# Performance work log

Hardware: AMD Instinct MI355X
Metric: run time of the kernel (lower is better)

Reference implementation:

```python
import jax, jax.numpy as jnp
import numpy as np

EMBED_DIM = 1024
NUM_HEADS = 16
HEAD_DIM = EMBED_DIM // NUM_HEADS


def setup_inputs() -> dict:
    key = jax.random.key(0)
    ks = jax.random.split(key, 10)
    B, S, D = 4, 2048, EMBED_DIM
    s = 1.0 / np.sqrt(D)
    return {
        "x": jax.random.normal(ks[0], (B, S, D), dtype=jnp.float32),
        "Wq": jax.random.normal(ks[1], (D, D), dtype=jnp.float32) * s,
        "bq": jnp.zeros((D,), dtype=jnp.float32),
        "Wk": jax.random.normal(ks[2], (D, D), dtype=jnp.float32) * s,
        "bk": jnp.zeros((D,), dtype=jnp.float32),
        "Wv": jax.random.normal(ks[3], (D, D), dtype=jnp.float32) * s,
        "bv": jnp.zeros((D,), dtype=jnp.float32),
        "Wo": jax.random.normal(ks[4], (D, D), dtype=jnp.float32) * s,
        "bo": jnp.zeros((D,), dtype=jnp.float32),
        "ln_w": jnp.ones((D,), dtype=jnp.float32),
        "ln_b": jnp.zeros((D,), dtype=jnp.float32),
    }


def _layernorm(x, w, b, eps=1e-5):
    mu = jnp.mean(x, axis=-1, keepdims=True)
    var = jnp.mean(jnp.square(x - mu), axis=-1, keepdims=True)
    return (x - mu) * jax.lax.rsqrt(var + eps) * w + b


def reference(x, Wq, bq, Wk, bk, Wv, bv, Wo, bo, ln_w, ln_b):
    B, S, D = x.shape
    H, hd = NUM_HEADS, HEAD_DIM
    # projections (torch Linear: x @ W.T + b)
    q = (x @ Wq.T + bq).reshape(B, S, H, hd).transpose(0, 2, 1, 3)  # [B,H,S,hd]
    k = (x @ Wk.T + bk).reshape(B, S, H, hd).transpose(0, 2, 1, 3)
    v = (x @ Wv.T + bv).reshape(B, S, H, hd).transpose(0, 2, 1, 3)
    scores = jnp.einsum("bhqd,bhkd->bhqk", q, k) / np.sqrt(hd)
    attn = jax.nn.softmax(scores, axis=-1)
    out = jnp.einsum("bhqk,bhkd->bhqd", attn, v)
    out = out.transpose(0, 2, 1, 3).reshape(B, S, D)
    out = out @ Wo.T + bo
    return _layernorm(out, ln_w, ln_b)
```

## Files before the change

kernel.cpp:

```cpp
#include <hip/hip_runtime.h>
#include <hip/hip_bf16.h>
#include <math.h>

typedef unsigned short u16;
typedef unsigned int   u32;
typedef short bf16x8 __attribute__((ext_vector_type(8)));
typedef float f32x4  __attribute__((ext_vector_type(4)));
typedef float f32x16 __attribute__((ext_vector_type(16)));
typedef u32   u32x4  __attribute__((ext_vector_type(4)));
typedef u32   u32x2  __attribute__((ext_vector_type(2)));

#define B_   4
#define S_   2048
#define D_   1024
#define H_   16
#define HD_  64
#define M_   (B_*S_)

static __device__ __forceinline__ u16 f2bf(float f) {
  __hip_bfloat16 h = __float2bfloat16(f);
  return *reinterpret_cast<u16*>(&h);
}
static __device__ __forceinline__ u32 pack_bf(float lo, float hi) {
  return (u32)f2bf(lo) | ((u32)f2bf(hi) << 16);
}
static __device__ __forceinline__ u32 pack_bf_trunc(float lo, float hi) {
  return __builtin_amdgcn_perm(__float_as_uint(hi), __float_as_uint(lo), 0x07060302u);
}
static __device__ __forceinline__ f32x16 zero16() {
  f32x16 z;
#pragma unroll
  for (int i = 0; i < 16; ++i) z[i] = 0.f;
  return z;
}

typedef __attribute__((address_space(1))) const u32* gas_t;
typedef __attribute__((address_space(3))) u32* las_t;
static __device__ __forceinline__ void g2l16(const void* g, void* l) {
  __builtin_amdgcn_global_load_lds((gas_t)g, (las_t)l, 16, 0, 0);
}

__global__ __launch_bounds__(256) void cast_all(const float* __restrict__ x,
                                                const float* __restrict__ Wq,
                                                const float* __restrict__ Wk,
                                                const float* __restrict__ Wv,
                                                const float* __restrict__ Wo,
                                                u16* __restrict__ xb,
                                                u16* __restrict__ Wqb,
                                                u16* __restrict__ Wkb,
                                                u16* __restrict__ Wvb,
                                                u16* __restrict__ Wob) {
  int bid = blockIdx.x;
  const float* src;
  u16* dst;
  int off;
  if (bid < 8192) {
    src = x; dst = xb; off = bid;
  } else {
    int t = bid - 8192;
    int w = t >> 10;
    off   = t & 1023;
    src = w == 0 ? Wq : w == 1 ? Wk : w == 2 ? Wv : Wo;
    dst = w == 0 ? Wqb : w == 1 ? Wkb : w == 2 ? Wvb : Wob;
  }
  int i = (off * 256 + threadIdx.x) * 4;
  float4 v = *reinterpret_cast<const float4*>(src + i);
  uint2 o;
  o.x = pack_bf(v.x, v.y);
  o.y = pack_bf(v.z, v.w);
  *reinterpret_cast<uint2*>(dst + i) = o;
}

__global__ __launch_bounds__(256) void gemm_qkv(const u16* __restrict__ A,
                                                const u16* __restrict__ Wq,
                                                const u16* __restrict__ Wk,
                                                const u16* __restrict__ Wv,
                                                const float* __restrict__ bq,
                                                const float* __restrict__ bk,
                                                const float* __restrict__ bv,
                                                u16* __restrict__ Qo,
                                                u16* __restrict__ Ko,
                                                u16* __restrict__ Vo) {
  const int tid  = threadIdx.x;
  const int lane = tid & 63;
  const int wave = tid >> 6;
  const int m16  = lane & 15;
  const int quad = lane >> 4;
  const int wm   = wave & 1;
  const int wn   = wave >> 1;
  const int which = blockIdx.x % 3;
  const int m0   = (blockIdx.x / 3) * 128;
  const int n0   = blockIdx.y * 128;

  const u16* W = which == 0 ? Wq : which == 1 ? Wk : Wv;
  const float* bias = which == 0 ? bq : which == 1 ? bk : bv;

  __shared__ __align__(16) u16 As[128 * 32];
  __shared__ __align__(16) u16 Bs[128 * 32];

  f32x4 acc[4][4];
#pragma unroll
  for (int i = 0; i < 4; ++i)
#pragma unroll
    for (int j = 0; j < 4; ++j) acc[i][j] = (f32x4){0.f, 0.f, 0.f, 0.f};

  for (int k0 = 0; k0 < 1024; k0 += 32) {
#pragma unroll
    for (int i = 0; i < 2; ++i) {
      int e0  = i * 256 + (wave << 6);
      int e   = e0 + lane;
      int row = e >> 2;
      int c8  = (e & 3) * 8;
      g2l16(&A[(size_t)(m0 + row) * 1024 + k0 + c8], &As[e0 * 8]);
      g2l16(&W[(size_t)(n0 + row) * 1024 + k0 + c8], &Bs[e0 * 8]);
    }
    __syncthreads();

    bf16x8 af[4], bfr[4];
#pragma unroll
    for (int mt = 0; mt < 4; ++mt)
      af[mt] = *reinterpret_cast<const bf16x8*>(&As[(wm * 64 + mt * 16 + m16) * 32 + quad * 8]);
#pragma unroll
    for (int nt = 0; nt < 4; ++nt)
      bfr[nt] = *reinterpret_cast<const bf16x8*>(&Bs[(wn * 64 + nt * 16 + m16) * 32 + quad * 8]);

#pragma unroll
    for (int mt = 0; mt < 4; ++mt)
#pragma unroll
      for (int nt = 0; nt < 4; ++nt)
        acc[mt][nt] = __builtin_amdgcn_mfma_f32_16x16x32_bf16(af[mt], bfr[nt], acc[mt][nt], 0, 0, 0);
    __syncthreads();
  }

  const float scale = which == 0 ? 0.125f * 1.44269504f : 1.0f;
  u16* ob = which == 0 ? Qo : which == 1 ? Ko : Vo;
#pragma unroll
  for (int mt = 0; mt < 4; ++mt) {
#pragma unroll
    for (int nt = 0; nt < 4; ++nt) {
      int col = n0 + wn * 64 + nt * 16 + m16;
      float bi = bias[col];
      int row0 = m0 + wm * 64 + mt * 16 + quad * 4;
      int b = row0 >> 11, s = row0 & 2047;
      int h = col >> 6,  d = col & 63;
      float v[4];
#pragma unroll
      for (int r = 0; r < 4; ++r) v[r] = (acc[mt][nt][r] + bi) * scale;
      if (which < 2) {
#pragma unroll
        for (int r = 0; r < 4; ++r)
          ob[(size_t)((b * H_ + h) * S_ + s + r) * HD_ + d] = f2bf(v[r]);
      } else {
        uint2 w;
        w.x = pack_bf(v[0], v[1]);
        w.y = pack_bf(v[2], v[3]);
        *reinterpret_cast<uint2*>(&ob[(size_t)((b * H_ + h) * HD_ + d) * S_ + s]) = w;
      }
    }
  }
}

__global__ __launch_bounds__(256) void gemm_bt(const u16* __restrict__ A,
                                               const u16* __restrict__ W,
                                               const float* __restrict__ bias,
                                               float* __restrict__ out) {
  const int tid  = threadIdx.x;
  const int lane = tid & 63;
  const int wave = tid >> 6;
  const int m16  = lane & 15;
  const int quad = lane >> 4;
  const int wm   = wave & 1;
  const int wn   = wave >> 1;
  const int m0   = blockIdx.x * 128;
  const int n0   = blockIdx.y * 128;

  __shared__ __align__(16) u16 As[128 * 32];
  __shared__ __align__(16) u16 Bs[128 * 32];

  f32x4 acc[4][4];
#pragma unroll
  for (int i = 0; i < 4; ++i)
#pragma unroll
    for (int j = 0; j < 4; ++j) acc[i][j] = (f32x4){0.f, 0.f, 0.f, 0.f};

  for (int k0 = 0; k0 < 1024; k0 += 32) {
#pragma unroll
    for (int i = 0; i < 2; ++i) {
      int e0  = i * 256 + (wave << 6);
      int e   = e0 + lane;
      int row = e >> 2;
      int c8  = (e & 3) * 8;
      g2l16(&A[(size_t)(m0 + row) * 1024 + k0 + c8], &As[e0 * 8]);
      g2l16(&W[(size_t)(n0 + row) * 1024 + k0 + c8], &Bs[e0 * 8]);
    }
    __syncthreads();

    bf16x8 af[4], bfr[4];
#pragma unroll
    for (int mt = 0; mt < 4; ++mt)
      af[mt] = *reinterpret_cast<const bf16x8*>(&As[(wm * 64 + mt * 16 + m16) * 32 + quad * 8]);
#pragma unroll
    for (int nt = 0; nt < 4; ++nt)
      bfr[nt] = *reinterpret_cast<const bf16x8*>(&Bs[(wn * 64 + nt * 16 + m16) * 32 + quad * 8]);

#pragma unroll
    for (int mt = 0; mt < 4; ++mt)
#pragma unroll
      for (int nt = 0; nt < 4; ++nt)
        acc[mt][nt] = __builtin_amdgcn_mfma_f32_16x16x32_bf16(af[mt], bfr[nt], acc[mt][nt], 0, 0, 0);
    __syncthreads();
  }

#pragma unroll
  for (int mt = 0; mt < 4; ++mt) {
#pragma unroll
    for (int nt = 0; nt < 4; ++nt) {
      int col = n0 + wn * 64 + nt * 16 + m16;
      float bi = bias[col];
#pragma unroll
      for (int r = 0; r < 4; ++r) {
        int row = m0 + wm * 64 + mt * 16 + quad * 4 + r;
        out[(size_t)row * 1024 + col] = acc[mt][nt][r] + bi;
      }
    }
  }
}

__global__ __launch_bounds__(256, 4) void attn_kernel(const u16* __restrict__ Q,
                                                      const u16* __restrict__ K,
                                                      const u16* __restrict__ Vt,
                                                      u16* __restrict__ out) {
  const int tid  = threadIdx.x;
  const int lane = tid & 63;
  const int wave = tid >> 6;
  const int r32  = lane & 31;
  const int h32  = lane >> 5;
  const int bh   = blockIdx.y;
  const int q0   = blockIdx.x * 128 + wave * 32;

  __shared__ __align__(16) u16 Ks[2][64 * 72];
  __shared__ __align__(16) u16 Vs[2][64 * 72];

  const u16* kbase = K  + (size_t)bh * S_ * HD_;
  const u16* vbase = Vt + (size_t)bh * HD_ * S_;
  const int e  = tid;
  const int e2 = tid + 256;
  const int row_a = e >> 3,  c8_a = (e & 7) * 8;
  const int row_b = e2 >> 3, c8_b = (e2 & 7) * 8;

  bf16x8 qf[4];
  {
    const u16* qbase = Q + (size_t)(bh * S_ + q0 + r32) * HD_ + h32 * 8;
#pragma unroll
    for (int dc = 0; dc < 4; ++dc)
      qf[dc] = *reinterpret_cast<const bf16x8*>(qbase + dc * 16);
  }

  f32x16 acc[2];
#pragma unroll
  for (int dt = 0; dt < 2; ++dt) acc[dt] = zero16();
  float lsum = 0.f;

  uint4 kr0 = *reinterpret_cast<const uint4*>(&kbase[(size_t)row_a * HD_ + c8_a]);
  uint4 kr1 = *reinterpret_cast<const uint4*>(&kbase[(size_t)row_b * HD_ + c8_b]);
  uint4 vr0 = *reinterpret_cast<const uint4*>(&vbase[(size_t)row_a * S_ + c8_a]);
  uint4 vr1 = *reinterpret_cast<const uint4*>(&vbase[(size_t)row_b * S_ + c8_b]);

  const int NT = S_ / 64;
  for (int kt = 0; kt < NT; ++kt) {
    u16* ks = Ks[kt & 1];
    u16* vs = Vs[kt & 1];
    *reinterpret_cast<uint4*>(&ks[row_a * 72 + c8_a]) = kr0;
    *reinterpret_cast<uint4*>(&ks[row_b * 72 + c8_b]) = kr1;
    *reinterpret_cast<uint4*>(&vs[row_a * 72 + c8_a]) = vr0;
    *reinterpret_cast<uint4*>(&vs[row_b * 72 + c8_b]) = vr1;
    __syncthreads();

    {
      const int kn = (kt + 1 < NT ? kt + 1 : kt) * 64;
      kr0 = *reinterpret_cast<const uint4*>(&kbase[(size_t)(kn + row_a) * HD_ + c8_a]);
      kr1 = *reinterpret_cast<const uint4*>(&kbase[(size_t)(kn + row_b) * HD_ + c8_b]);
      vr0 = *reinterpret_cast<const uint4*>(&vbase[(size_t)row_a * S_ + kn + c8_a]);
      vr1 = *reinterpret_cast<const uint4*>(&vbase[(size_t)row_b * S_ + kn + c8_b]);
    }

    f32x16 sc[2];
    __builtin_amdgcn_s_setprio(1);
#pragma unroll
    for (int nt = 0; nt < 2; ++nt) {
      sc[nt] = zero16();
#pragma unroll
      for (int dc = 0; dc < 4; ++dc) {
        bf16x8 kf = *reinterpret_cast<const bf16x8*>(&ks[(nt * 32 + r32) * 72 + dc * 16 + h32 * 8]);
        sc[nt] = __builtin_amdgcn_mfma_f32_32x32x16_bf16(kf, qf[dc], sc[nt], 0, 0, 0);
      }
    }
    __builtin_amdgcn_s_setprio(0);

    u32 pk[2][8];
    float ps0 = 0.f, ps1 = 0.f;
#pragma unroll
    for (int nt = 0; nt < 2; ++nt)
#pragma unroll
      for (int i = 0; i < 8; ++i) {
        float p0 = __builtin_amdgcn_exp2f(sc[nt][2 * i]);
        float p1 = __builtin_amdgcn_exp2f(sc[nt][2 * i + 1]);
        ps0 += p0;
        ps1 += p1;
        pk[nt][i] = pack_bf_trunc(p0, p1);
      }
    lsum += ps0 + ps1;

    __builtin_amdgcn_s_setprio(1);
#pragma unroll
    for (int nt = 0; nt < 2; ++nt) {
#pragma unroll
      for (int kc2 = 0; kc2 < 2; ++kc2) {
        u32x2 r0 = __builtin_amdgcn_permlane32_swap(pk[nt][4 * kc2 + 0], pk[nt][4 * kc2 + 2], false, false);
        u32x2 r1 = __builtin_amdgcn_permlane32_swap(pk[nt][4 * kc2 + 1], pk[nt][4 * kc2 + 3], false, false);
        u32x4 bw;
        bw[0] = r0[0];
        bw[1] = r1[0];
        bw[2] = r0[1];
        bw[3] = r1[1];
        bf16x8 pfrag = *reinterpret_cast<bf16x8*>(&bw);
        const int kc = nt * 2 + kc2;
#pragma unroll
        for (int dt = 0; dt < 2; ++dt) {
          bf16x8 vf = *reinterpret_cast<const bf16x8*>(&vs[(dt * 32 + r32) * 72 + kc * 16 + h32 * 8]);
          acc[dt] = __builtin_amdgcn_mfma_f32_32x32x16_bf16(vf, pfrag, acc[dt], 0, 0, 0);
        }
      }
    }
    __builtin_amdgcn_s_setprio(0);
  }

  const int b = bh >> 4, hh = bh & 15;
  float lt  = lsum + __shfl_xor(lsum, 32);
  float inv = 1.f / lt;
  int srow = q0 + r32;
  u16* orow = out + (size_t)(b * S_ + srow) * D_ + hh * HD_;
#pragma unroll
  for (int dt = 0; dt < 2; ++dt) {
#pragma unroll
    for (int g = 0; g < 4; ++g) {
      uint2 w;
      w.x = pack_bf(acc[dt][4 * g + 0] * inv, acc[dt][4 * g + 1] * inv);
      w.y = pack_bf(acc[dt][4 * g + 2] * inv, acc[dt][4 * g + 3] * inv);
      *reinterpret_cast<uint2*>(orow + dt * 32 + 8 * g + 4 * h32) = w;
    }
  }
}

__global__ __launch_bounds__(256) void ln_kernel(const float* __restrict__ X,
                                                 const float* __restrict__ w,
                                                 const float* __restrict__ b,
                                                 float* __restrict__ out) {
  const int row = blockIdx.x;
  const int tid = threadIdx.x;
  const float* x = X + (size_t)row * 1024;
  float vals[4];
  float s = 0.f, s2 = 0.f;
#pragma unroll
  for (int i = 0; i < 4; ++i) {
    float v = x[tid + i * 256];
    vals[i] = v;
    s += v;
    s2 += v * v;
  }
#pragma unroll
  for (int off = 32; off; off >>= 1) {
    s  += __shfl_xor(s, off);
    s2 += __shfl_xor(s2, off);
  }
  __shared__ float a1[4], a2[4];
  if ((tid & 63) == 0) { a1[tid >> 6] = s; a2[tid >> 6] = s2; }
  __syncthreads();
  s  = a1[0] + a1[1] + a1[2] + a1[3];
  s2 = a2[0] + a2[1] + a2[2] + a2[3];
  float mu  = s * (1.f / 1024.f);
  float var = s2 * (1.f / 1024.f) - mu * mu;
  float inv = rsqrtf(var + 1e-5f);
#pragma unroll
  for (int i = 0; i < 4; ++i) {
    int c = tid + i * 256;
    out[(size_t)row * 1024 + c] = (vals[i] - mu) * inv * w[c] + b[c];
  }
}

extern "C" void kernel_launch(void* const* d_in, const int* in_sizes, int n_in,
                              void* d_out, int out_size, void* d_ws, size_t ws_size,
                              hipStream_t stream) {
  const float* x   = (const float*)d_in[0];
  const float* Wq  = (const float*)d_in[1];
  const float* bq  = (const float*)d_in[2];
  const float* Wk  = (const float*)d_in[3];
  const float* bk  = (const float*)d_in[4];
  const float* Wv  = (const float*)d_in[5];
  const float* bv  = (const float*)d_in[6];
  const float* Wo  = (const float*)d_in[7];
  const float* bo  = (const float*)d_in[8];
  const float* lnw = (const float*)d_in[9];
  const float* lnb = (const float*)d_in[10];

  const size_t MB = 1024ull * 1024ull;
  char* ws = (char*)d_ws;
  u16* xb  = (u16*)(ws + 0);
  u16* Qb  = (u16*)(ws + 16 * MB);
  u16* Kb  = (u16*)(ws + 32 * MB);
  u16* Vtb = (u16*)(ws + 48 * MB);
  u16* Wqb = (u16*)(ws + 64 * MB);
  u16* Wkb = (u16*)(ws + 66 * MB);
  u16* Wvb = (u16*)(ws + 68 * MB);
  u16* Wob = (u16*)(ws + 70 * MB);
  float* Of = (float*)(ws + 16 * MB);

  cast_all<<<8192 + 4096, 256, 0, stream>>>(x, Wq, Wk, Wv, Wo, xb, Wqb, Wkb, Wvb, Wob);

  gemm_qkv<<<dim3((M_ / 128) * 3, D_ / 128), 256, 0, stream>>>(
      xb, Wqb, Wkb, Wvb, bq, bk, bv, Qb, Kb, Vtb);

  attn_kernel<<<dim3(S_ / 128, B_ * H_), 256, 0, stream>>>(Qb, Kb, Vtb, xb);

  gemm_bt<<<dim3(M_ / 128, D_ / 128), 256, 0, stream>>>(xb, Wob, bo, Of);

  ln_kernel<<<M_, 256, 0, stream>>>(Of, lnw, lnb, (float*)d_out);
}
```

Measured before the change: 304.5 us.

## Double-buffer GEMM LDS tiles and swizzle block order for XCD locality

Both projection GEMMs now use two LDS buffers, so the global-to-LDS copy of the next K tile is issued before computing on the current one, overlapping loads with MFMA work and dropping one barrier per iteration. All three kernels switch to 1D grids with a block-index swizzle (bid&7 striding), which groups neighbouring tiles onto the same XCD to improve L2 reuse of A/W and K/V. This doubles LDS use in the GEMMs, which may reduce occupancy.

Result: slower. 320.9 us (+5.4%).

```diff
diff --git a/kernel.cpp b/kernel.cpp
--- a/kernel.cpp
+++ b/kernel.cpp
@@ -88,15 +88,21 @@
   const int quad = lane >> 4;
   const int wm   = wave & 1;
   const int wn   = wave >> 1;
-  const int which = blockIdx.x % 3;
-  const int m0   = (blockIdx.x / 3) * 128;
-  const int n0   = blockIdx.y * 128;
+
+  const int bid = blockIdx.x;
+  const int swz = (bid & 7) * 192 + (bid >> 3);
+  const int m_   = swz / 24;
+  const int rr   = swz % 24;
+  const int which = rr >> 3;
+  const int nb   = rr & 7;
+  const int m0   = m_ * 128;
+  const int n0   = nb * 128;
 
   const u16* W = which == 0 ? Wq : which == 1 ? Wk : Wv;
   const float* bias = which == 0 ? bq : which == 1 ? bk : bv;
 
-  __shared__ __align__(16) u16 As[128 * 32];
-  __shared__ __align__(16) u16 Bs[128 * 32];
+  __shared__ __align__(16) u16 As[2][128 * 32];
+  __shared__ __align__(16) u16 Bs[2][128 * 32];
 
   f32x4 acc[4][4];
 #pragma unroll
@@ -104,25 +110,33 @@
 #pragma unroll
     for (int j = 0; j < 4; ++j) acc[i][j] = (f32x4){0.f, 0.f, 0.f, 0.f};
 
-  for (int k0 = 0; k0 < 1024; k0 += 32) {
-#pragma unroll
-    for (int i = 0; i < 2; ++i) {
-      int e0  = i * 256 + (wave << 6);
-      int e   = e0 + lane;
-      int row = e >> 2;
-      int c8  = (e & 3) * 8;
-      g2l16(&A[(size_t)(m0 + row) * 1024 + k0 + c8], &As[e0 * 8]);
-      g2l16(&W[(size_t)(n0 + row) * 1024 + k0 + c8], &Bs[e0 * 8]);
-    }
-    __syncthreads();
+#define QKV_STAGE(buf, k0)                                                   \
+  {                                                                          \
+    _Pragma("unroll")                                                        \
+    for (int i = 0; i < 2; ++i) {                                            \
+      int e0  = i * 256 + (wave << 6);                                       \
+      int e   = e0 + lane;                                                   \
+      int row = e >> 2;                                                      \
+      int c8  = (e & 3) * 8;                                                 \
+      g2l16(&A[(size_t)(m0 + row) * 1024 + (k0) + c8], &As[buf][e0 * 8]);    \
+      g2l16(&W[(size_t)(n0 + row) * 1024 + (k0) + c8], &Bs[buf][e0 * 8]);    \
+    }                                                                        \
+  }
+
+  QKV_STAGE(0, 0);
+  __syncthreads();
+
+  for (int t = 0; t < 32; ++t) {
+    const int cur = t & 1;
+    if (t + 1 < 32) QKV_STAGE(cur ^ 1, (t + 1) * 32);
 
     bf16x8 af[4], bfr[4];
 #pragma unroll
     for (int mt = 0; mt < 4; ++mt)
-      af[mt] = *reinterpret_cast<const bf16x8*>(&As[(wm * 64 + mt * 16 + m16) * 32 + quad * 8]);
+      af[mt] = *reinterpret_cast<const bf16x8*>(&As[cur][(wm * 64 + mt * 16 + m16) * 32 + quad * 8]);
 #pragma unroll
     for (int nt = 0; nt < 4; ++nt)
-      bfr[nt] = *reinterpret_cast<const bf16x8*>(&Bs[(wn * 64 + nt * 16 + m16) * 32 + quad * 8]);
+      bfr[nt] = *reinterpret_cast<const bf16x8*>(&Bs[cur][(wn * 64 + nt * 16 + m16) * 32 + quad * 8]);
 
 #pragma unroll
     for (int mt = 0; mt < 4; ++mt)
@@ -131,6 +145,7 @@
         acc[mt][nt] = __builtin_amdgcn_mfma_f32_16x16x32_bf16(af[mt], bfr[nt], acc[mt][nt], 0, 0, 0);
     __syncthreads();
   }
+#undef QKV_STAGE
 
   const float scale = which == 0 ? 0.125f * 1.44269504f : 1.0f;
   u16* ob = which == 0 ? Qo : which == 1 ? Ko : Vo;
@@ -171,11 +186,14 @@
   const int quad = lane >> 4;
   const int wm   = wave & 1;
   const int wn   = wave >> 1;
-  const int m0   = blockIdx.x * 128;
-  const int n0   = blockIdx.y * 128;
-
-  __shared__ __align__(16) u16 As[128 * 32];
-  __shared__ __align__(16) u16 Bs[128 * 32];
+
+  const int bid = blockIdx.x;
+  const int swz = (bid & 7) * 64 + (bid >> 3);
+  const int m0  = (swz >> 3) * 128;
+  const int n0  = (swz & 7) * 128;
+
+  __shared__ __align__(16) u16 As[2][128 * 32];
+  __shared__ __align__(16) u16 Bs[2][128 * 32];
 
   f32x4 acc[4][4];
 #pragma unroll
@@ -183,25 +201,33 @@
 #pragma unroll
     for (int j = 0; j < 4; ++j) acc[i][j] = (f32x4){0.f, 0.f, 0.f, 0.f};
 
-  for (int k0 = 0; k0 < 1024; k0 += 32) {
-#pragma unroll
-    for (int i = 0; i < 2; ++i) {
-      int e0  = i * 256 + (wave << 6);
-      int e   = e0 + lane;
-      int row = e >> 2;
-      int c8  = (e & 3) * 8;
-      g2l16(&A[(size_t)(m0 + row) * 1024 + k0 + c8], &As[e0 * 8]);
-      g2l16(&W[(size_t)(n0 + row) * 1024 + k0 + c8], &Bs[e0 * 8]);
-    }
-    __syncthreads();
+#define BT_STAGE(buf, k0)                                                    \
+  {                                                                          \
+    _Pragma("unroll")                                                        \
+    for (int i = 0; i < 2; ++i) {                                            \
+      int e0  = i * 256 + (wave << 6);                                       \
+      int e   = e0 + lane;                                                   \
+      int row = e >> 2;                                                      \
+      int c8  = (e & 3) * 8;                                                 \
+      g2l16(&A[(size_t)(m0 + row) * 1024 + (k0) + c8], &As[buf][e0 * 8]);    \
+      g2l16(&W[(size_t)(n0 + row) * 1024 + (k0) + c8], &Bs[buf][e0 * 8]);    \
+    }                                                                        \
+  }
+
+  BT_STAGE(0, 0);
+  __syncthreads();
+
+  for (int t = 0; t < 32; ++t) {
+    const int cur = t & 1;
+    if (t + 1 < 32) BT_STAGE(cur ^ 1, (t + 1) * 32);
 
     bf16x8 af[4], bfr[4];
 #pragma unroll
     for (int mt = 0; mt < 4; ++mt)
-      af[mt] = *reinterpret_cast<const bf16x8*>(&As[(wm * 64 + mt * 16 + m16) * 32 + quad * 8]);
+      af[mt] = *reinterpret_cast<const bf16x8*>(&As[cur][(wm * 64 + mt * 16 + m16) * 32 + quad * 8]);
 #pragma unroll
     for (int nt = 0; nt < 4; ++nt)
-      bfr[nt] = *reinterpret_cast<const bf16x8*>(&Bs[(wn * 64 + nt * 16 + m16) * 32 + quad * 8]);
+      bfr[nt] = *reinterpret_cast<const bf16x8*>(&Bs[cur][(wn * 64 + nt * 16 + m16) * 32 + quad * 8]);
 
 #pragma unroll
     for (int mt = 0; mt < 4; ++mt)
@@ -210,6 +236,7 @@
         acc[mt][nt] = __builtin_amdgcn_mfma_f32_16x16x32_bf16(af[mt], bfr[nt], acc[mt][nt], 0, 0, 0);
     __syncthreads();
   }
+#undef BT_STAGE
 
 #pragma unroll
   for (int mt = 0; mt < 4; ++mt) {
@@ -235,8 +262,11 @@
   const int wave = tid >> 6;
   const int r32  = lane & 31;
   const int h32  = lane >> 5;
-  const int bh   = blockIdx.y;
-  const int q0   = blockIdx.x * 128 + wave * 32;
+
+  const int bid = blockIdx.x;
+  const int swz = (bid & 7) * 128 + (bid >> 3);
+  const int bh  = swz >> 4;
+  const int q0  = (swz & 15) * 128 + wave * 32;
 
   __shared__ __align__(16) u16 Ks[2][64 * 72];
   __shared__ __align__(16) u16 Vs[2][64 * 72];
@@ -417,12 +447,12 @@
 
   cast_all<<<8192 + 4096, 256, 0, stream>>>(x, Wq, Wk, Wv, Wo, xb, Wqb, Wkb, Wvb, Wob);
 
-  gemm_qkv<<<dim3((M_ / 128) * 3, D_ / 128), 256, 0, stream>>>(
+  gemm_qkv<<<(M_ / 128) * 3 * (D_ / 128), 256, 0, stream>>>(
       xb, Wqb, Wkb, Wvb, bq, bk, bv, Qb, Kb, Vtb);
 
-  attn_kernel<<<dim3(S_ / 128, B_ * H_), 256, 0, stream>>>(Qb, Kb, Vtb, xb);
-
-  gemm_bt<<<dim3(M_ / 128, D_ / 128), 256, 0, stream>>>(xb, Wob, bo, Of);
+  attn_kernel<<<(S_ / 128) * B_ * H_, 256, 0, stream>>>(Qb, Kb, Vtb, xb);
+
+  gemm_bt<<<(M_ / 128) * (D_ / 128), 256, 0, stream>>>(xb, Wob, bo, Of);
 
   ln_kernel<<<M_, 256, 0, stream>>>(Of, lnw, lnb, (float*)d_out);
 }
```
